# Kernel tuning notes

Hardware: AMD Instinct MI355X
Metric: run time of the kernel (lower is better)

The kernel has to match this reference:

```python
import jax, jax.numpy as jnp
import numpy as np

N_RAYS, N_SAMPLES, WIDTH = 4096, 192, 128


def _linear_params(key, fan_in, fan_out):
    # torch nn.Linear default init: U(-1/sqrt(fan_in), 1/sqrt(fan_in))
    kw, kb = jax.random.split(key)
    s = 1.0 / np.sqrt(fan_in)
    w = jax.random.uniform(kw, (fan_in, fan_out), minval=-s, maxval=s, dtype=jnp.float32)
    b = jax.random.uniform(kb, (fan_out,), minval=-s, maxval=s, dtype=jnp.float32)
    return w, b


def setup_inputs() -> dict:
    key = jax.random.key(0)
    ks = jax.random.split(key, 9)
    w0, b0 = _linear_params(ks[0], 3, WIDTH)            # feature layer 0
    w1, b1 = _linear_params(ks[1], WIDTH, WIDTH)        # feature layer 1
    w2, b2 = _linear_params(ks[2], WIDTH + 3, WIDTH)    # feature layer 2 (skip concat)
    w3, b3 = _linear_params(ks[3], WIDTH, WIDTH)        # feature layer 3
    wd, bd = _linear_params(ks[4], WIDTH, 1)            # density head
    wf, bf = _linear_params(ks[5], WIDTH, WIDTH)        # feature head
    wr, br = _linear_params(ks[6], WIDTH + 3, WIDTH // 2)  # rgb layer
    wo, bo = _linear_params(ks[7], WIDTH // 2, 3)       # rgb head
    x = jax.random.normal(ks[8], (N_RAYS, N_SAMPLES, 6), dtype=jnp.float32)
    return dict(x=x, w0=w0, b0=b0, w1=w1, b1=b1, w2=w2, b2=b2, w3=w3, b3=b3,
                wd=wd, bd=bd, wf=wf, bf=bf, wr=wr, br=br, wo=wo, bo=bo)


def reference(x, w0, b0, w1, b1, w2, b2, w3, b3, wd, bd, wf, bf, wr, br, wo, bo):
    relu = jax.nn.relu
    position, view_dir = x[..., :3], x[..., 3:]
    h = relu(position @ w0 + b0)                                   # [R,S,128]
    h = relu(h @ w1 + b1)
    h = relu(jnp.concatenate([h, position], axis=-1) @ w2 + b2)    # skip at i=2
    h = relu(h @ w3 + b3)
    density = relu(h @ wd + bd)                                    # [R,S,1]
    features = relu(h @ wf + bf)                                   # [R,S,128]
    r = relu(jnp.concatenate([features, view_dir], axis=-1) @ wr + br)  # [R,S,64]
    rgb = jax.nn.sigmoid(r @ wo + bo)                              # [R,S,3]
    return (rgb, density)
```

## Files before the change

kernel.cpp:

```cpp
#include <hip/hip_runtime.h>
#include <hip/hip_bf16.h>

#define N_PTS (4096 * 192)
#define NT    4

typedef __bf16 bf16x8 __attribute__((ext_vector_type(8)));
typedef float  f32x4  __attribute__((ext_vector_type(4)));
typedef float  f32x2  __attribute__((ext_vector_type(2)));

#define W1P 0
#define W2P 16384
#define W3P 32768
#define WFP 49152
#define WRP 65536
#define W0E 73728
#define W2E 75776
#define WRE 77824
#define WDE 78848
#define WOE 79104
#define WMAIN_ELEMS 73728

__device__ __forceinline__ int kinv(int k) {
  int c = k >> 5, q = (k >> 3) & 3, h = (k >> 2) & 1, r = k & 3;
  return (2 * c + h) * 16 + q * 4 + r;
}

__global__ void prep_kernel(const float* __restrict__ w0, const float* __restrict__ w1,
                            const float* __restrict__ w2, const float* __restrict__ w3,
                            const float* __restrict__ wf, const float* __restrict__ wr,
                            const float* __restrict__ wd, const float* __restrict__ wo,
                            __bf16* __restrict__ ws) {
  int i = blockIdx.x * 256 + threadIdx.x;
  if (i < 65536) {
    int t = i >> 14, j = i & 16383, m = j >> 7, col = j & 127;
    int k = (((col >> 3) ^ (m & 15)) << 3) | (col & 7);
    int p = kinv(k);
    const float* w = (t == 0) ? w1 : (t == 1) ? w2 : (t == 2) ? w3 : wf;
    ws[i] = (__bf16)w[p * 128 + m];
  } else if (i < 73728) {
    int j = i - 65536, m = j >> 7, col = j & 127;
    int k = (((col >> 3) ^ (m & 15)) << 3) | (col & 7);
    ws[i] = (__bf16)wr[kinv(k) * 64 + m];
  } else if (i < 75776) {
    int j = i - 73728, f = j >> 4, k = j & 15; float v = 0.f;
    if (k < 3)      v = w0[k * 128 + f];
    else if (k < 6) v = w0[(k - 3) * 128 + f];
    else if (k < 9) { float w = w0[(k - 6) * 128 + f]; v = w - (float)(__bf16)w; }
    ws[i] = (__bf16)v;
  } else if (i < 77824) {
    int j = i - 75776, f = j >> 4, k = j & 15; float v = 0.f;
    if (k < 3)      v = w2[(128 + k) * 128 + f];
    else if (k < 6) v = w2[(128 + k - 3) * 128 + f];
    else if (k < 9) { float w = w2[(128 + k - 6) * 128 + f]; v = w - (float)(__bf16)w; }
    ws[i] = (__bf16)v;
  } else if (i < 78848) {
    int j = i - 77824, n = j >> 4, k = j & 15; float v = 0.f;
    if (k >= 9 && k < 15) v = wr[(128 + ((k - 9) % 3)) * 64 + n];
    ws[i] = (__bf16)v;
  } else if (i < 79104) {
    int j = i - 78848, row = j >> 7, k = j & 127, p = kinv(k);
    float v = wd[p];
    ws[i] = (row == 0) ? (__bf16)v : (__bf16)(v - (float)(__bf16)v);
  } else if (i < 79616) {
    int j = i - 79104, row = j >> 6, k = j & 63, p = kinv(k);
    float v = 0.f;
    if (row < 3)                 v = wo[p * 3 + row];
    else if (row >= 4 && row < 7) { float w = wo[p * 3 + row - 4]; v = w - (float)(__bf16)w; }
    ws[i] = (__bf16)v;
  }
}

__device__ __forceinline__ bf16x8 zero8() {
  bf16x8 z;
#pragma unroll
  for (int i = 0; i < 8; ++i) z[i] = (__bf16)0.f;
  return z;
}

__device__ __forceinline__ bf16x8 pack_relu(f32x4 e, f32x4 o) {
  bf16x8 v;
#pragma unroll
  for (int r = 0; r < 4; ++r) {
    v[r]     = (__bf16)fmaxf(e[r], 0.f);
    v[4 + r] = (__bf16)fmaxf(o[r], 0.f);
  }
  return v;
}

template <int NPAIR, bool FIX>
__device__ __forceinline__ void mlayer(const __bf16* __restrict__ wlds,
                                       const float* __restrict__ bias,
                                       const __bf16* __restrict__ wext,
                                       const bf16x8 (&pf)[NT],
                                       const bf16x8 (&hin)[4][NT],
                                       bf16x8 (&hout)[NPAIR][NT],
                                       const int (&lane_off)[4],
                                       int l16, int quad) {
#pragma unroll
  for (int pr = 0; pr < NPAIR; ++pr) {
    f32x4 acc0[NT], acc1[NT];
    f32x4 bv0 = *(const f32x4*)(bias + pr * 32 + quad * 4);
    f32x4 bv1 = *(const f32x4*)(bias + pr * 32 + 16 + quad * 4);
#pragma unroll
    for (int nt = 0; nt < NT; ++nt) { acc0[nt] = bv0; acc1[nt] = bv1; }
#pragma unroll
    for (int c = 0; c < 4; ++c) {
      const __bf16* base = wlds + pr * 4096 + lane_off[c];
      bf16x8 a0 = *(const bf16x8*)(base);
      bf16x8 a1 = *(const bf16x8*)(base + 2048);
#pragma unroll
      for (int nt = 0; nt < NT; ++nt) {
        acc0[nt] = __builtin_amdgcn_mfma_f32_16x16x32_bf16(a0, hin[c][nt], acc0[nt], 0, 0, 0);
        acc1[nt] = __builtin_amdgcn_mfma_f32_16x16x32_bf16(a1, hin[c][nt], acc1[nt], 0, 0, 0);
      }
    }
    if constexpr (FIX) {
      bf16x8 a0 = zero8(), a1 = zero8();
      if (quad < 2) {
        a0 = *(const bf16x8*)(wext + (pr * 32 + l16) * 16 + quad * 8);
        a1 = *(const bf16x8*)(wext + (pr * 32 + 16 + l16) * 16 + quad * 8);
      }
#pragma unroll
      for (int nt = 0; nt < NT; ++nt) {
        acc0[nt] = __builtin_amdgcn_mfma_f32_16x16x32_bf16(a0, pf[nt], acc0[nt], 0, 0, 0);
        acc1[nt] = __builtin_amdgcn_mfma_f32_16x16x32_bf16(a1, pf[nt], acc1[nt], 0, 0, 0);
      }
    }
#pragma unroll
    for (int nt = 0; nt < NT; ++nt) hout[pr][nt] = pack_relu(acc0[nt], acc1[nt]);
  }
}

__global__ __launch_bounds__(768)
__attribute__((amdgpu_waves_per_eu(2, 2)))
void nerf_kernel(
    const float* __restrict__ x,
    const float* __restrict__ b0, const float* __restrict__ b1,
    const float* __restrict__ b2, const float* __restrict__ b3,
    const float* __restrict__ bd, const float* __restrict__ bfv,
    const float* __restrict__ br, const float* __restrict__ bo,
    const __bf16* __restrict__ ws,
    float* __restrict__ out) {
  __shared__ __align__(16) __bf16 wsl[WMAIN_ELEMS];

  const int tid  = threadIdx.x;
  const int wv   = tid >> 6;
  const int lane = tid & 63;
  const int quad = lane >> 4;
  const int l16  = lane & 15;
  const int p0   = blockIdx.x * 768;
  const int pw   = wv * 64;

  f32x2 xr[NT][3];
  {
    const float* xp0 = x + (size_t)(p0 + pw) * 6;
#pragma unroll
    for (int nt = 0; nt < NT; ++nt) {
      const float* xp = xp0 + (nt * 16 + l16) * 6;
      xr[nt][0] = *(const f32x2*)xp;
      xr[nt][1] = *(const f32x2*)(xp + 2);
      xr[nt][2] = *(const f32x2*)(xp + 4);
    }
  }
  bf16x8 w0a[4], w0b[4];
#pragma unroll
  for (int pr = 0; pr < 4; ++pr) {
    w0a[pr] = zero8(); w0b[pr] = zero8();
    if (quad < 2) {
      w0a[pr] = *(const bf16x8*)(ws + W0E + (pr * 32 + l16) * 16 + quad * 8);
      w0b[pr] = *(const bf16x8*)(ws + W0E + (pr * 32 + 16 + l16) * 16 + quad * 8);
    }
  }

  {
    const char* g = (const char*)ws;
    char* l = (char*)wsl;
#pragma unroll
    for (int r = 0; r < 147456; r += 12288) {
      const char* src = g + r + wv * 1024 + lane * 16;
      char* dst = l + r + wv * 1024;
      __builtin_amdgcn_global_load_lds(
          (const __attribute__((address_space(1))) void*)src,
          (__attribute__((address_space(3))) void*)dst, 16, 0, 0);
    }
  }

  int lane_off[4];
#pragma unroll
  for (int c = 0; c < 4; ++c)
    lane_off[c] = l16 * 128 + ((((c * 4 + quad) ^ l16)) << 3);

  bf16x8 pf[NT];
#pragma unroll
  for (int nt = 0; nt < NT; ++nt) {
    float px = xr[nt][0][0], py = xr[nt][0][1], pz = xr[nt][1][0];
    float vx = xr[nt][1][1], vy = xr[nt][2][0], vz = xr[nt][2][1];
    bf16x8 v = zero8();
    if (quad == 0) {
      __bf16 phx = (__bf16)px, phy = (__bf16)py, phz = (__bf16)pz;
      v[0] = phx; v[1] = phy; v[2] = phz;
      v[3] = (__bf16)(px - (float)phx);
      v[4] = (__bf16)(py - (float)phy);
      v[5] = (__bf16)(pz - (float)phz);
      v[6] = phx; v[7] = phy;
    } else if (quad == 1) {
      __bf16 vhx = (__bf16)vx, vhy = (__bf16)vy, vhz = (__bf16)vz;
      v[0] = (__bf16)pz; v[1] = vhx; v[2] = vhy; v[3] = vhz;
      v[4] = (__bf16)(vx - (float)vhx);
      v[5] = (__bf16)(vy - (float)vhy);
      v[6] = (__bf16)(vz - (float)vhz);
      v[7] = (__bf16)0.f;
    }
    pf[nt] = v;
  }

  bf16x8 hA[4][NT], hB[4][NT];

#pragma unroll
  for (int pr = 0; pr < 4; ++pr) {
    f32x4 acc0[NT], acc1[NT];
    f32x4 bv0 = *(const f32x4*)(b0 + pr * 32 + quad * 4);
    f32x4 bv1 = *(const f32x4*)(b0 + pr * 32 + 16 + quad * 4);
#pragma unroll
    for (int nt = 0; nt < NT; ++nt) { acc0[nt] = bv0; acc1[nt] = bv1; }
#pragma unroll
    for (int nt = 0; nt < NT; ++nt) {
      acc0[nt] = __builtin_amdgcn_mfma_f32_16x16x32_bf16(w0a[pr], pf[nt], acc0[nt], 0, 0, 0);
      acc1[nt] = __builtin_amdgcn_mfma_f32_16x16x32_bf16(w0b[pr], pf[nt], acc1[nt], 0, 0, 0);
    }
#pragma unroll
    for (int nt = 0; nt < NT; ++nt) hA[pr][nt] = pack_relu(acc0[nt], acc1[nt]);
  }
  __syncthreads();

  mlayer<4, false>(wsl + W1P, b1, nullptr,   pf, hA, hB, lane_off, l16, quad);
  mlayer<4, true >(wsl + W2P, b2, ws + W2E,  pf, hB, hA, lane_off, l16, quad);
  mlayer<4, false>(wsl + W3P, b3, nullptr,   pf, hA, hB, lane_off, l16, quad);

  {
    f32x4 accd[NT];
#pragma unroll
    for (int nt = 0; nt < NT; ++nt) accd[nt] = f32x4{0.f, 0.f, 0.f, 0.f};
    int drow = (l16 < 2) ? l16 : 0;
#pragma unroll
    for (int c = 0; c < 4; ++c) {
      bf16x8 ad = *(const bf16x8*)(ws + WDE + drow * 128 + c * 32 + quad * 8);
#pragma unroll
      for (int nt = 0; nt < NT; ++nt)
        accd[nt] = __builtin_amdgcn_mfma_f32_16x16x32_bf16(ad, hB[c][nt], accd[nt], 0, 0, 0);
    }
    float bdv = bd[0];
    if (quad == 0) {
#pragma unroll
      for (int nt = 0; nt < NT; ++nt)
        out[(size_t)3 * N_PTS + p0 + pw + nt * 16 + l16] =
            fmaxf(accd[nt][0] + accd[nt][1] + bdv, 0.f);
    }
  }

  mlayer<4, false>(wsl + WFP, bfv, nullptr, pf, hB, hA, lane_off, l16, quad);

  bf16x8 hR[2][NT];
  mlayer<2, true>(wsl + WRP, br, ws + WRE, pf, hA, hR, lane_off, l16, quad);

  {
    f32x4 acco[NT];
#pragma unroll
    for (int nt = 0; nt < NT; ++nt) acco[nt] = f32x4{0.f, 0.f, 0.f, 0.f};
    int orow = l16 & 7;
#pragma unroll
    for (int c = 0; c < 2; ++c) {
      bf16x8 ao = *(const bf16x8*)(ws + WOE + orow * 64 + c * 32 + quad * 8);
#pragma unroll
      for (int nt = 0; nt < NT; ++nt)
        acco[nt] = __builtin_amdgcn_mfma_f32_16x16x32_bf16(ao, hR[c][nt], acco[nt], 0, 0, 0);
    }
    float bo0 = bo[0], bo1 = bo[1], bo2 = bo[2];
#pragma unroll
    for (int nt = 0; nt < NT; ++nt) {
      float lo0 = __shfl_xor(acco[nt][0], 16, 64);
      float lo1 = __shfl_xor(acco[nt][1], 16, 64);
      float lo2 = __shfl_xor(acco[nt][2], 16, 64);
      if (quad == 0) {
        size_t o = (size_t)(p0 + pw + nt * 16 + l16) * 3;
        out[o + 0] = 1.f / (1.f + __expf(-(acco[nt][0] + lo0 + bo0)));
        out[o + 1] = 1.f / (1.f + __expf(-(acco[nt][1] + lo1 + bo1)));
        out[o + 2] = 1.f / (1.f + __expf(-(acco[nt][2] + lo2 + bo2)));
      }
    }
  }
}

extern "C" void kernel_launch(void* const* d_in, const int* in_sizes, int n_in,
                              void* d_out, int out_size, void* d_ws, size_t ws_size,
                              hipStream_t stream) {
  const float* x  = (const float*)d_in[0];
  const float* w0 = (const float*)d_in[1];
  const float* b0 = (const float*)d_in[2];
  const float* w1 = (const float*)d_in[3];
  const float* b1 = (const float*)d_in[4];
  const float* w2 = (const float*)d_in[5];
  const float* b2 = (const float*)d_in[6];
  const float* w3 = (const float*)d_in[7];
  const float* b3 = (const float*)d_in[8];
  const float* wd = (const float*)d_in[9];
  const float* bd = (const float*)d_in[10];
  const float* wf = (const float*)d_in[11];
  const float* bfv= (const float*)d_in[12];
  const float* wr = (const float*)d_in[13];
  const float* br = (const float*)d_in[14];
  const float* wo = (const float*)d_in[15];
  const float* bo = (const float*)d_in[16];
  __bf16* ws = (__bf16*)d_ws;
  float* out = (float*)d_out;

  prep_kernel<<<311, 256, 0, stream>>>(w0, w1, w2, w3, wf, wr, wd, wo, ws);
  nerf_kernel<<<N_PTS / 768, 768, 0, stream>>>(x, b0, b1, b2, b3, bd, bfv, br, bo, ws, out);
}
```

Baseline: 250.0 us.

## Stream layer weights through two double-buffered LDS tiles with smaller blocks

Instead of loading all MLP weight matrices into one large LDS buffer before any compute, the kernel now keeps two 32 KB LDS tiles. While one layer computes on one tile, the next layer's weights are loaded asynchronously into the other. Blocks shrink from 768 to 384 threads and launch bounds are set for two blocks per CU, so independent blocks can overlap their load and compute phases. The trade-off is extra barriers between layers and twice as many weight fetches per point from L2.

```diff
diff --git a/kernel.cpp b/kernel.cpp
--- a/kernel.cpp
+++ b/kernel.cpp
@@ -18,7 +18,6 @@
 #define WRE 77824
 #define WDE 78848
 #define WOE 79104
-#define WMAIN_ELEMS 73728
 
 __device__ __forceinline__ int kinv(int k) {
   int c = k >> 5, q = (k >> 3) & 3, h = (k >> 2) & 1, r = k & 3;
@@ -87,6 +86,24 @@
   return v;
 }
 
+template <int NB>
+__device__ __forceinline__ void stage_tile(const __bf16* __restrict__ gsrc,
+                                           __bf16* lds, int wv, int lane) {
+  const char* g = (const char*)gsrc;
+  char* l = (char*)lds;
+#pragma unroll
+  for (int r = 0; r < NB; r += 6144) {
+    int off = r + wv * 1024;
+    if (off < NB) {
+      const char* src = g + off + lane * 16;
+      char* dst = l + off;
+      __builtin_amdgcn_global_load_lds(
+          (const __attribute__((address_space(1))) void*)src,
+          (__attribute__((address_space(3))) void*)dst, 16, 0, 0);
+    }
+  }
+}
+
 template <int NPAIR, bool FIX>
 __device__ __forceinline__ void mlayer(const __bf16* __restrict__ wlds,
                                        const float* __restrict__ bias,
@@ -131,9 +148,7 @@
   }
 }
 
-__global__ __launch_bounds__(768)
-__attribute__((amdgpu_waves_per_eu(2, 2)))
-void nerf_kernel(
+__global__ __launch_bounds__(384, 2) void nerf_kernel(
     const float* __restrict__ x,
     const float* __restrict__ b0, const float* __restrict__ b1,
     const float* __restrict__ b2, const float* __restrict__ b3,
@@ -141,15 +156,18 @@
     const float* __restrict__ br, const float* __restrict__ bo,
     const __bf16* __restrict__ ws,
     float* __restrict__ out) {
-  __shared__ __align__(16) __bf16 wsl[WMAIN_ELEMS];
-
+  __shared__ __align__(16) __bf16 sA[128 * 128];
+  __shared__ __align__(16) __bf16 sB[128 * 128];
   const int tid  = threadIdx.x;
   const int wv   = tid >> 6;
   const int lane = tid & 63;
   const int quad = lane >> 4;
   const int l16  = lane & 15;
-  const int p0   = blockIdx.x * 768;
+  const int p0   = blockIdx.x * 384;
   const int pw   = wv * 64;
+
+  stage_tile<32768>(ws + W1P, sA, wv, lane);
+  stage_tile<32768>(ws + W2P, sB, wv, lane);
 
   f32x2 xr[NT][3];
   {
@@ -169,19 +187,6 @@
     if (quad < 2) {
       w0a[pr] = *(const bf16x8*)(ws + W0E + (pr * 32 + l16) * 16 + quad * 8);
       w0b[pr] = *(const bf16x8*)(ws + W0E + (pr * 32 + 16 + l16) * 16 + quad * 8);
-    }
-  }
-
-  {
-    const char* g = (const char*)ws;
-    char* l = (char*)wsl;
-#pragma unroll
-    for (int r = 0; r < 147456; r += 12288) {
-      const char* src = g + r + wv * 1024 + lane * 16;
-      char* dst = l + r + wv * 1024;
-      __builtin_amdgcn_global_load_lds(
-          (const __attribute__((address_space(1))) void*)src,
-          (__attribute__((address_space(3))) void*)dst, 16, 0, 0);
     }
   }
 
@@ -233,9 +238,17 @@
   }
   __syncthreads();
 
-  mlayer<4, false>(wsl + W1P, b1, nullptr,   pf, hA, hB, lane_off, l16, quad);
-  mlayer<4, true >(wsl + W2P, b2, ws + W2E,  pf, hB, hA, lane_off, l16, quad);
-  mlayer<4, false>(wsl + W3P, b3, nullptr,   pf, hA, hB, lane_off, l16, quad);
+  mlayer<4, false>(sA, b1, nullptr, pf, hA, hB, lane_off, l16, quad);
+  __syncthreads();
+  stage_tile<32768>(ws + W3P, sA, wv, lane);
+
+  mlayer<4, true>(sB, b2, ws + W2E, pf, hB, hA, lane_off, l16, quad);
+  __syncthreads();
+  stage_tile<32768>(ws + WFP, sB, wv, lane);
+
+  mlayer<4, false>(sA, b3, nullptr, pf, hA, hB, lane_off, l16, quad);
+  __syncthreads();
+  stage_tile<16384>(ws + WRP, sA, wv, lane);
 
   {
     f32x4 accd[NT];
@@ -258,10 +271,11 @@
     }
   }
 
-  mlayer<4, false>(wsl + WFP, bfv, nullptr, pf, hB, hA, lane_off, l16, quad);
+  mlayer<4, false>(sB, bfv, nullptr, pf, hB, hA, lane_off, l16, quad);
+  __syncthreads();
 
   bf16x8 hR[2][NT];
-  mlayer<2, true>(wsl + WRP, br, ws + WRE, pf, hA, hR, lane_off, l16, quad);
+  mlayer<2, true>(sA, br, ws + WRE, pf, hA, hR, lane_off, l16, quad);
 
   {
     f32x4 acco[NT];
@@ -315,5 +329,5 @@
   float* out = (float*)d_out;
 
   prep_kernel<<<311, 256, 0, stream>>>(w0, w1, w2, w3, wf, wr, wd, wo, ws);
-  nerf_kernel<<<N_PTS / 768, 768, 0, stream>>>(x, b0, b1, b2, b3, bd, bfv, br, bo, ws, out);
-}
+  nerf_kernel<<<N_PTS / 384, 384, 0, stream>>>(x, b0, b1, b2, b3, bd, bfv, br, bo, ws, out);
+}
```

New measurement: 244.7 us. -2.1%, faster.
